# Kernel optimization log

Hardware: AMD Instinct MI355X
Metric: run time of the kernel (lower is better)

## Reference

```python
import jax, jax.numpy as jnp
import numpy as np

D, H, L, FF, V, B, S = 512, 8, 6, 2048, 4096, 2, 4096
EPS = 1e-5

def _unit(v):
    return v / jnp.linalg.norm(v, axis=-1, keepdims=True)

def _unitelu(v):
    return jax.nn.elu(_unit(v))

def _ln(x, g, b):
    m = jnp.mean(x, axis=-1, keepdims=True)
    var = jnp.var(x, axis=-1, keepdims=True)
    return (x - m) * jax.lax.rsqrt(var + EPS) * g + b

def setup_inputs() -> dict:
    key = jax.random.key(0)
    ks = jax.random.split(key, 16)
    s = 0.02
    inp = {
        'input': jax.random.randint(ks[0], (B, S), 0, V),
        'emb': jax.random.normal(ks[1], (V, D)) * s,
        'Wq': jax.random.normal(ks[2], (L, D, D)) * s,
        'bq': jnp.zeros((L, D)),
        'Wk': jax.random.normal(ks[3], (L, D, D)) * s,
        'bk': jnp.zeros((L, D)),
        'Wv': jax.random.normal(ks[4], (L, D, D)) * s,
        'bv': jnp.zeros((L, D)),
        'Wo': jax.random.normal(ks[5], (L, D, D)) * s,
        'bo': jnp.zeros((L, D)),
        'W1': jax.random.normal(ks[6], (L, FF, D)) * s,
        'b1': jnp.zeros((L, FF)),
        'W2': jax.random.normal(ks[7], (L, D, FF)) * s,
        'b2': jnp.zeros((L, D)),
        'g2': jnp.ones((L, D)),
        'be2': jnp.zeros((L, D)),
        'Wfc': jax.random.normal(ks[8], (V, D)) * s,
        'bfc': jnp.zeros((V,)),
    }
    return inp

def reference(input, emb, Wq, bq, Wk, bk, Wv, bv, Wo, bo, W1, b1, W2, b2, g2, be2, Wfc, bfc):
    # h: [S, B, D] (seq-major, matching input.permute(1,0) then embedding)
    h = emb[input.T]
    for l in range(L):
        # linear kernelized attention: O(S * dh^2) per head, no SxS matrix
        k = _unitelu((h @ Wk[l].T + bk[l]).reshape(S, B, H, -1))  # [S,B,H,dh]
        v = (h @ Wv[l].T + bv[l]).reshape(S, B, H, -1)
        A = jnp.einsum('sbnq,sbnv->bnvq', k, v)                    # [B,H,dh,dh]
        q = _unit((h @ Wq[l].T + bq[l]).reshape(S, B, H, -1))
        o = jnp.einsum('sbnq,bnvq->sbnv', q, A).reshape(S, B, D)
        h = h + (o @ Wo[l].T + bo[l])
        f = jax.nn.relu(h @ W1[l].T + b1[l]) @ W2[l].T + b2[l]
        h = _ln(h + f, g2[l], be2[l])
    out = h @ Wfc.T + bfc          # [S, B, V]
    return out.transpose(1, 2, 0)  # [B, V, S]
```

## Files before the change

kernel.cpp:

```cpp
#include <hip/hip_runtime.h>
#include <hip/hip_bf16.h>

#define D_  512
#define H_  8
#define DH_ 64
#define L_  6
#define FF_ 2048
#define V_  4096
#define B_  2
#define S_  4096
#define SB_ (S_*B_)
#define DD_ ((size_t)D_*D_)
#define FD_ ((size_t)FF_*D_)
#define NTOT_ (4*DD_ + 2*FD_)

typedef unsigned short u16;
typedef unsigned int   u32;
typedef _Float16 f16;
typedef f16   f16x8 __attribute__((ext_vector_type(8)));
typedef float f32x4 __attribute__((ext_vector_type(4)));

__device__ __forceinline__ float us2f(u16 u){
  union { u32 i; float f; } c; c.i = ((u32)u) << 16; return c.f;
}
__device__ __forceinline__ u16 f2b(float f){
  union { float f; u32 i; } c; c.f = f;
  u32 x = c.i;
  x += 0x7FFF + ((x >> 16) & 1);
  return (u16)(x >> 16);
}
__device__ __forceinline__ float h2f(u16 u){
  union { u16 s; f16 h; } c; c.s = u; return (float)c.h;
}
__device__ __forceinline__ u16 f2h(float f){
  union { f16 h; u16 s; } c; c.h = (f16)f; return c.s;
}
__device__ __forceinline__ float ldf(const void* p, size_t i, int isbf){
  return isbf ? us2f(((const u16*)p)[i]) : ((const float*)p)[i];
}

typedef const __attribute__((address_space(1))) u32* gas_u32p;
typedef       __attribute__((address_space(3))) u32* las_u32p;
__device__ __forceinline__ void async16(const u16* g, u16* l){
  __builtin_amdgcn_global_load_lds((gas_u32p)(const void*)g, (las_u32p)(void*)l, 16, 0, 0);
}

__global__ __launch_bounds__(64) void detect_dtype(const void* emb, int* flag)
{
  const int t = threadIdx.x;
  u16 hw = ((const u16*)emb)[t];
  int e = (hw >> 7) & 0xFF;
  int ok = ((e > 96) && (e < 160)) || ((hw & 0x7FFF) == 0);
  unsigned long long m = __ballot(ok);
  if (t == 0) *flag = (__popcll(m) >= 56) ? 1 : 0;
}

__global__ __launch_bounds__(256) void cvt_all(
    const void* Wq, const void* Wk, const void* Wv, const void* Wo,
    const void* W1, const void* W2, const void* Wfc,
    u16* __restrict__ dstAll, u16* __restrict__ dstFC, const int* flagp)
{
  const int isbf = *flagp;
  const size_t total6 = 6 * NTOT_;
  const size_t i = ((size_t)blockIdx.x * 256 + threadIdx.x) * 4;
  const void* src; size_t off; u16* dst;
  if (i < total6) {
    const int l = (int)(i / NTOT_);
    const size_t r = i - (size_t)l * NTOT_;
    const size_t n4 = 4 * DD_, nW1 = n4 + FD_;
    if (r < n4) {
      const int wsel = (int)(r / DD_);
      src = (wsel == 0) ? Wq : (wsel == 1) ? Wk : (wsel == 2) ? Wv : Wo;
      off = (size_t)l * DD_ + (r - (size_t)wsel * DD_);
    } else if (r < nW1) { src = W1; off = (size_t)l * FD_ + (r - n4); }
    else                { src = W2; off = (size_t)l * FD_ + (r - nW1); }
    dst = dstAll + i;
  } else {
    const size_t j = i - total6;
    if (j >= (size_t)V_ * D_) return;
    src = Wfc; off = j; dst = dstFC + j;
  }
  ushort4 o;
  if (isbf) {
    ushort4 u = *(const ushort4*)((const u16*)src + off);
    o = make_ushort4(f2h(us2f(u.x)), f2h(us2f(u.y)), f2h(us2f(u.z)), f2h(us2f(u.w)));
  } else {
    float4 f = *(const float4*)((const float*)src + off);
    o = make_ushort4(f2h(f.x), f2h(f.y), f2h(f.z), f2h(f.w));
  }
  *(ushort4*)dst = o;
}

template<int ACT, int OUTMODE, int PRE>
__global__ __launch_bounds__(256) void gemm_mfma(
    const u16* __restrict__ A, const u16* __restrict__ Bm,
    int bstride, int boff,
    const void* bias, size_t bias_off,
    const float* __restrict__ res,
    float* __restrict__ Cf, u16* __restrict__ Cb,
    void* __restrict__ Cout,
    int M, int N, int K, const int* flagp)
{
  __shared__ u16 tile[(PRE + 1) * 8192];
  const int t = threadIdx.x, lane = t & 63, w = t >> 6;
  const int bm = blockIdx.y << 7, bn = blockIdx.x << 7;
  const int bz = blockIdx.z;
  const int wr = w >> 1, wc = w & 1;
  const int col = lane & 15, quad = lane >> 4;

  const int srow = w * 16 + (lane >> 2);
  const int skol = (((lane & 3) ^ ((lane >> 3) & 3)) << 3);
  const u16* ag0 = A + (size_t)(bm + srow) * K + skol;
  const u16* ag1 = A + (size_t)(bm + 64 + srow) * K + skol;
  const u16* bg0 = Bm + ((size_t)(bn + srow) * bstride + boff + bz) * K + skol;
  const u16* bg1 = Bm + ((size_t)(bn + 64 + srow) * bstride + boff + bz) * K + skol;
  u16* la0 = &tile[       w * 512];
  u16* la1 = &tile[2048 + w * 512];
  u16* lb0 = &tile[4096 + w * 512];
  u16* lb1 = &tile[6144 + w * 512];

  const int nt = K >> 5;

  #pragma unroll
  for (int p = 0; p < PRE; ++p) {
    const int k0 = p << 5, bo = p * 8192;
    async16(ag0 + k0, la0 + bo);
    async16(ag1 + k0, la1 + bo);
    async16(bg0 + k0, lb0 + bo);
    async16(bg1 + k0, lb1 + bo);
  }
  if      (PRE >= 3) asm volatile("s_waitcnt vmcnt(8)" ::: "memory");
  else if (PRE == 2) asm volatile("s_waitcnt vmcnt(4)" ::: "memory");
  else               asm volatile("s_waitcnt vmcnt(0)" ::: "memory");
  __builtin_amdgcn_s_barrier();
  asm volatile("" ::: "memory");

  const int rswz = ((col >> 1) & 3);

  f32x4 acc[4][4] = {};
  for (int t2 = 0; t2 < nt; ++t2) {
    if (t2 + PRE < nt) {
      const int k0 = (t2 + PRE) << 5;
      const int bo = ((t2 + PRE) % (PRE + 1)) * 8192;
      async16(ag0 + k0, la0 + bo);
      async16(ag1 + k0, la1 + bo);
      async16(bg0 + k0, lb0 + bo);
      async16(bg1 + k0, lb1 + bo);
    }
    const int cur = (t2 % (PRE + 1)) * 8192;
    f16x8 af[4], bf[4];
    #pragma unroll
    for (int i = 0; i < 4; i++)
      af[i] = *(const f16x8*)&tile[cur + (wr * 64 + i * 16 + col) * 32 + ((quad ^ rswz) * 8)];
    #pragma unroll
    for (int j = 0; j < 4; j++)
      bf[j] = *(const f16x8*)&tile[cur + 4096 + (wc * 64 + j * 16 + col) * 32 + ((quad ^ rswz) * 8)];
    #pragma unroll
    for (int i = 0; i < 4; i++)
      #pragma unroll
      for (int j = 0; j < 4; j++)
        acc[i][j] = __builtin_amdgcn_mfma_f32_16x16x32_f16(af[i], bf[j], acc[i][j], 0, 0, 0);
    if (PRE >= 3) {
      if      (t2 + 3 < nt) asm volatile("s_waitcnt vmcnt(8)" ::: "memory");
      else if (t2 + 2 < nt) asm volatile("s_waitcnt vmcnt(4)" ::: "memory");
      else                  asm volatile("s_waitcnt vmcnt(0)" ::: "memory");
    } else if (PRE == 2) {
      if (t2 + 2 < nt) asm volatile("s_waitcnt vmcnt(4)" ::: "memory");
      else             asm volatile("s_waitcnt vmcnt(0)" ::: "memory");
    } else {
      asm volatile("s_waitcnt vmcnt(0)" ::: "memory");
    }
    __builtin_amdgcn_s_barrier();
    asm volatile("" ::: "memory");
  }

  const int isbf = *flagp;
  #pragma unroll
  for (int i = 0; i < 4; i++) {
    #pragma unroll
    for (int r = 0; r < 4; r++) {
      const int m = bm + wr * 64 + i * 16 + quad * 4 + r;
      #pragma unroll
      for (int j = 0; j < 4; j++) {
        const int n = bn + wc * 64 + j * 16 + col;
        float c = acc[i][j][r];
        if (OUTMODE == 3) c += ldf(bias, bias_off + m, isbf);
        else              c += ldf(bias, bias_off + n, isbf);
        if (res) c += res[(size_t)m * N + n];
        if (ACT == 1) c = fmaxf(c, 0.f);
        if (OUTMODE == 0) {
          Cb[(size_t)m * N + n] = f2h(c);
        } else if (OUTMODE == 1) {
          Cf[(size_t)m * N + n] = c;
          Cb[(size_t)m * N + n] = f2h(c);
        } else {
          const size_t oi = (size_t)bz * M * N + (size_t)m * N + n;
          if (isbf) ((u16*)Cout)[oi] = f2b(c);
          else      ((float*)Cout)[oi] = c;
        }
      }
    }
  }
}

template<int ACT, int OUTMODE, int PRE>
__global__ __launch_bounds__(256) void gemm_mfma64(
    const u16* __restrict__ A, const u16* __restrict__ Bm,
    const void* bias, size_t bias_off,
    const float* __restrict__ res,
    float* __restrict__ Cf, u16* __restrict__ Cb,
    int M, int N, int K, const int* flagp)
{
  __shared__ u16 tile[(PRE + 1) * 6144];
  const int t = threadIdx.x, lane = t & 63, w = t >> 6;
  const int bm = blockIdx.y << 6, bn = blockIdx.x << 7;
  const int wr = w >> 1, wc = w & 1;
  const int col = lane & 15, quad = lane >> 4;

  const int srow = w * 16 + (lane >> 2);
  const int skol = (((lane & 3) ^ ((lane >> 3) & 3)) << 3);
  const u16* ag  = A + (size_t)(bm + srow) * K + skol;
  const u16* bg0 = Bm + (size_t)(bn + srow) * K + skol;
  const u16* bg1 = Bm + (size_t)(bn + 64 + srow) * K + skol;
  u16* la  = &tile[       w * 512];
  u16* lb0 = &tile[2048 + w * 512];
  u16* lb1 = &tile[4096 + w * 512];

  const int nt = K >> 5;

  #pragma unroll
  for (int p = 0; p < PRE; ++p) {
    const int k0 = p << 5, bo = p * 6144;
    async16(ag  + k0, la  + bo);
    async16(bg0 + k0, lb0 + bo);
    async16(bg1 + k0, lb1 + bo);
  }
  if      (PRE >= 3) asm volatile("s_waitcnt vmcnt(6)" ::: "memory");
  else if (PRE == 2) asm volatile("s_waitcnt vmcnt(3)" ::: "memory");
  else               asm volatile("s_waitcnt vmcnt(0)" ::: "memory");
  __builtin_amdgcn_s_barrier();
  asm volatile("" ::: "memory");

  const int rswz = ((col >> 1) & 3);

  f32x4 acc[2][4] = {};
  for (int t2 = 0; t2 < nt; ++t2) {
    if (t2 + PRE < nt) {
      const int k0 = (t2 + PRE) << 5;
      const int bo = ((t2 + PRE) % (PRE + 1)) * 6144;
      async16(ag  + k0, la  + bo);
      async16(bg0 + k0, lb0 + bo);
      async16(bg1 + k0, lb1 + bo);
    }
    const int cur = (t2 % (PRE + 1)) * 6144;
    f16x8 af[2], bf[4];
    #pragma unroll
    for (int i = 0; i < 2; i++)
      af[i] = *(const f16x8*)&tile[cur + (wr * 32 + i * 16 + col) * 32 + ((quad ^ rswz) * 8)];
    #pragma unroll
    for (int j = 0; j < 4; j++)
      bf[j] = *(const f16x8*)&tile[cur + 2048 + (wc * 64 + j * 16 + col) * 32 + ((quad ^ rswz) * 8)];
    #pragma unroll
    for (int i = 0; i < 2; i++)
      #pragma unroll
      for (int j = 0; j < 4; j++)
        acc[i][j] = __builtin_amdgcn_mfma_f32_16x16x32_f16(af[i], bf[j], acc[i][j], 0, 0, 0);
    if (PRE >= 3) {
      if      (t2 + 3 < nt) asm volatile("s_waitcnt vmcnt(6)" ::: "memory");
      else if (t2 + 2 < nt) asm volatile("s_waitcnt vmcnt(3)" ::: "memory");
      else                  asm volatile("s_waitcnt vmcnt(0)" ::: "memory");
    } else if (PRE == 2) {
      if (t2 + 2 < nt) asm volatile("s_waitcnt vmcnt(3)" ::: "memory");
      else             asm volatile("s_waitcnt vmcnt(0)" ::: "memory");
    } else {
      asm volatile("s_waitcnt vmcnt(0)" ::: "memory");
    }
    __builtin_amdgcn_s_barrier();
    asm volatile("" ::: "memory");
  }

  const int isbf = *flagp;
  #pragma unroll
  for (int i = 0; i < 2; i++) {
    #pragma unroll
    for (int r = 0; r < 4; r++) {
      const int m = bm + wr * 32 + i * 16 + quad * 4 + r;
      #pragma unroll
      for (int j = 0; j < 4; j++) {
        const int n = bn + wc * 64 + j * 16 + col;
        float c = acc[i][j][r] + ldf(bias, bias_off + n, isbf);
        if (res) c += res[(size_t)m * N + n];
        if (ACT == 1) c = fmaxf(c, 0.f);
        if (OUTMODE == 0) {
          Cb[(size_t)m * N + n] = f2h(c);
        } else {
          Cf[(size_t)m * N + n] = c;
          Cb[(size_t)m * N + n] = f2h(c);
        }
      }
    }
  }
}

__global__ __launch_bounds__(256) void gemm_qkv(
    const u16* __restrict__ A, const u16* __restrict__ Bm,
    const void* bq, const void* bk, const void* bv, size_t b_off,
    u16* __restrict__ qb, u16* __restrict__ kb, u16* __restrict__ vb,
    int K, const int* flagp)
{
  __shared__ u16 tile[3 * 8192];
  const int t = threadIdx.x, lane = t & 63, w = t >> 6;
  const int bm = blockIdx.y << 7, bn = blockIdx.x << 7;
  const int wr = w >> 1, wc = w & 1;
  const int col = lane & 15, quad = lane >> 4;

  const int srow = w * 16 + (lane >> 2);
  const int skol = (((lane & 3) ^ ((lane >> 3) & 3)) << 3);
  const u16* ag0 = A + (size_t)(bm + srow) * K + skol;
  const u16* ag1 = A + (size_t)(bm + 64 + srow) * K + skol;
  const u16* bg0 = Bm + (size_t)(bn + srow) * K + skol;
  const u16* bg1 = Bm + (size_t)(bn + 64 + srow) * K + skol;
  u16* la0 = &tile[       w * 512];
  u16* la1 = &tile[2048 + w * 512];
  u16* lb0 = &tile[4096 + w * 512];
  u16* lb1 = &tile[6144 + w * 512];

  const int nt = K >> 5;

  #pragma unroll
  for (int p = 0; p < 2; ++p) {
    const int k0 = p << 5, bo = p * 8192;
    async16(ag0 + k0, la0 + bo);
    async16(ag1 + k0, la1 + bo);
    async16(bg0 + k0, lb0 + bo);
    async16(bg1 + k0, lb1 + bo);
  }
  asm volatile("s_waitcnt vmcnt(4)" ::: "memory");
  __builtin_amdgcn_s_barrier();
  asm volatile("" ::: "memory");

  const int rswz = ((col >> 1) & 3);

  f32x4 acc[4][4] = {};
  for (int t2 = 0; t2 < nt; ++t2) {
    if (t2 + 2 < nt) {
      const int k0 = (t2 + 2) << 5;
      const int bo = ((t2 + 2) % 3) * 8192;
      async16(ag0 + k0, la0 + bo);
      async16(ag1 + k0, la1 + bo);
      async16(bg0 + k0, lb0 + bo);
      async16(bg1 + k0, lb1 + bo);
    }
    const int cur = (t2 % 3) * 8192;
    f16x8 af[4], bf[4];
    #pragma unroll
    for (int i = 0; i < 4; i++)
      af[i] = *(const f16x8*)&tile[cur + (wr * 64 + i * 16 + col) * 32 + ((quad ^ rswz) * 8)];
    #pragma unroll
    for (int j = 0; j < 4; j++)
      bf[j] = *(const f16x8*)&tile[cur + 4096 + (wc * 64 + j * 16 + col) * 32 + ((quad ^ rswz) * 8)];
    #pragma unroll
    for (int i = 0; i < 4; i++)
      #pragma unroll
      for (int j = 0; j < 4; j++)
        acc[i][j] = __builtin_amdgcn_mfma_f32_16x16x32_f16(af[i], bf[j], acc[i][j], 0, 0, 0);
    if (t2 + 2 < nt) asm volatile("s_waitcnt vmcnt(4)" ::: "memory");
    else             asm volatile("s_waitcnt vmcnt(0)" ::: "memory");
    __builtin_amdgcn_s_barrier();
    asm volatile("" ::: "memory");
  }

  const int isbf = *flagp;
  const int nbase = bn + wc * 64;
  const int sel = nbase >> 9;
  const int nl0 = nbase & 511;
  u16* outp = (sel == 0) ? qb : (sel == 1) ? kb : vb;
  const void* bias = (sel == 0) ? bq : (sel == 1) ? bk : bv;

  if (sel < 2) {
    #pragma unroll
    for (int i = 0; i < 4; i++) {
      #pragma unroll
      for (int r = 0; r < 4; r++) {
        float v[4]; float ss = 0.f;
        #pragma unroll
        for (int j = 0; j < 4; j++) {
          const int nl = nl0 + j * 16 + col;
          v[j] = acc[i][j][r] + ldf(bias, b_off + nl, isbf);
          ss += v[j] * v[j];
        }
        ss += __shfl_xor(ss, 1); ss += __shfl_xor(ss, 2);
        ss += __shfl_xor(ss, 4); ss += __shfl_xor(ss, 8);
        const float inv = rsqrtf(fmaxf(ss, 1e-30f));
        const int m = bm + wr * 64 + i * 16 + quad * 4 + r;
        #pragma unroll
        for (int j = 0; j < 4; j++) {
          float u = v[j] * inv;
          if (sel == 1) u = (u > 0.f) ? u : expm1f(u);
          outp[(size_t)m * 512 + nl0 + j * 16 + col] = f2h(u);
        }
      }
    }
  } else {
    #pragma unroll
    for (int i = 0; i < 4; i++)
      #pragma unroll
      for (int r = 0; r < 4; r++) {
        const int m = bm + wr * 64 + i * 16 + quad * 4 + r;
        #pragma unroll
        for (int j = 0; j < 4; j++) {
          const int nl = nl0 + j * 16 + col;
          outp[(size_t)m * 512 + nl] = f2h(acc[i][j][r] + ldf(bias, b_off + nl, isbf));
        }
      }
  }
}

#define KT_ 136
__global__ __launch_bounds__(256) void attn_acc_mfma(
    const u16* __restrict__ kbuf, const u16* __restrict__ vbuf,
    float* __restrict__ Apart)
{
  __shared__ u16 ktr[64 * KT_];
  __shared__ u16 vtr[64 * KT_];
  const int bh = blockIdx.x;
  const int b  = bh >> 3, n = bh & 7;
  const int s0 = blockIdx.y << 7;
  const int t = threadIdx.x, lane = t & 63, w = t >> 6;
  const int col = lane & 15, quad = lane >> 4;

  #pragma unroll
  for (int u = 0; u < 8; u++) {
    const int flat = u * 256 + t;
    const int row = flat >> 4, q4 = (flat & 15) << 2;
    const size_t g = ((size_t)(s0 + row) * B_ + b) * D_ + n * 64 + q4;
    ushort4 kk = *(const ushort4*)&kbuf[g];
    ushort4 vv = *(const ushort4*)&vbuf[g];
    ktr[(q4+0)*KT_ + row] = kk.x; ktr[(q4+1)*KT_ + row] = kk.y;
    ktr[(q4+2)*KT_ + row] = kk.z; ktr[(q4+3)*KT_ + row] = kk.w;
    vtr[(q4+0)*KT_ + row] = vv.x; vtr[(q4+1)*KT_ + row] = vv.y;
    vtr[(q4+2)*KT_ + row] = vv.z; vtr[(q4+3)*KT_ + row] = vv.w;
  }
  __syncthreads();

  f32x4 acc[4] = {};
  #pragma unroll
  for (int ks = 0; ks < 4; ks++) {
    const int k0 = ks * 32;
    f16x8 af = *(const f16x8*)&vtr[(w * 16 + col) * KT_ + k0 + quad * 8];
    #pragma unroll
    for (int j = 0; j < 4; j++) {
      f16x8 bf = *(const f16x8*)&ktr[(j * 16 + col) * KT_ + k0 + quad * 8];
      acc[j] = __builtin_amdgcn_mfma_f32_16x16x32_f16(af, bf, acc[j], 0, 0, 0);
    }
  }
  float* Ap = Apart + ((size_t)blockIdx.y * 16 + bh) * 4096;
  #pragma unroll
  for (int j = 0; j < 4; j++)
    #pragma unroll
    for (int r = 0; r < 4; r++) {
      const int vi = w * 16 + quad * 4 + r, qi = j * 16 + col;
      Ap[vi * 64 + qi] = acc[j][r];
    }
}

__global__ __launch_bounds__(256) void reduce_A(
    const float* __restrict__ Apart, u16* __restrict__ Ah)
{
  const int i = blockIdx.x * 256 + threadIdx.x;
  const int bh = i >> 12, idx = i & 4095;
  float s = 0.f;
  #pragma unroll
  for (int p = 0; p < 32; p++)
    s += Apart[((size_t)p * 16 + bh) * 4096 + idx];
  Ah[i] = f2h(s);
}

__global__ __launch_bounds__(256) void attn_apply_mfma(
    u16* __restrict__ qo, const u16* __restrict__ Ah)
{
  const int bh = blockIdx.x;
  const int b = bh >> 3, n = bh & 7;
  const int s0 = blockIdx.y << 7;
  const int t = threadIdx.x, lane = t & 63, w = t >> 6;
  const int col = lane & 15, quad = lane >> 4;

  const u16* Ab_ = Ah + (size_t)bh * 4096;
  f16x8 bf[4][2];
  #pragma unroll
  for (int j = 0; j < 4; j++)
    #pragma unroll
    for (int ks = 0; ks < 2; ks++)
      bf[j][ks] = *(const f16x8*)&Ab_[(j * 16 + col) * 64 + ks * 32 + quad * 8];

  const int srow_base = s0 + w * 32;
  f32x4 acc[2][4] = {};
  #pragma unroll
  for (int i = 0; i < 2; i++) {
    const int s = srow_base + i * 16 + col;
    const u16* qp = qo + ((size_t)s * B_ + b) * D_ + n * 64;
    f16x8 af0 = *(const f16x8*)&qp[quad * 8];
    f16x8 af1 = *(const f16x8*)&qp[32 + quad * 8];
    #pragma unroll
    for (int j = 0; j < 4; j++) {
      acc[i][j] = __builtin_amdgcn_mfma_f32_16x16x32_f16(af0, bf[j][0], acc[i][j], 0, 0, 0);
      acc[i][j] = __builtin_amdgcn_mfma_f32_16x16x32_f16(af1, bf[j][1], acc[i][j], 0, 0, 0);
    }
  }
  #pragma unroll
  for (int i = 0; i < 2; i++)
    #pragma unroll
    for (int r = 0; r < 4; r++) {
      const int s = srow_base + i * 16 + quad * 4 + r;
      u16* op = qo + ((size_t)s * B_ + b) * D_ + n * 64;
      #pragma unroll
      for (int j = 0; j < 4; j++)
        op[j * 16 + col] = f2h(acc[i][j][r]);
    }
}

__global__ __launch_bounds__(256) void ln_k(
    float* __restrict__ h, u16* __restrict__ hb,
    const void* g, size_t g_off, const void* be, size_t be_off, const int* flagp)
{
  const int isbf = *flagp;
  const int m = blockIdx.x, t = threadIdx.x;
  float* p = h + (size_t)m * D_;
  const float x0 = p[t], x1 = p[t + 256];
  __shared__ float red[4];
  float s = x0 + x1;
  #pragma unroll
  for (int off = 32; off >= 1; off >>= 1) s += __shfl_xor(s, off);
  if ((t & 63) == 0) red[t >> 6] = s;
  __syncthreads();
  const float mean = (red[0] + red[1] + red[2] + red[3]) * (1.f / 512.f);
  const float d0 = x0 - mean, d1 = x1 - mean;
  float s2 = d0 * d0 + d1 * d1;
  #pragma unroll
  for (int off = 32; off >= 1; off >>= 1) s2 += __shfl_xor(s2, off);
  __syncthreads();
  if ((t & 63) == 0) red[t >> 6] = s2;
  __syncthreads();
  const float var = (red[0] + red[1] + red[2] + red[3]) * (1.f / 512.f);
  const float sc = rsqrtf(var + 1e-5f);
  const float y0 = d0 * sc * ldf(g, g_off + t, isbf)       + ldf(be, be_off + t, isbf);
  const float y1 = d1 * sc * ldf(g, g_off + t + 256, isbf) + ldf(be, be_off + t + 256, isbf);
  p[t] = y0;       p[t + 256] = y1;
  hb[(size_t)m * D_ + t] = f2h(y0);
  hb[(size_t)m * D_ + t + 256] = f2h(y1);
}

__global__ __launch_bounds__(512) void embed_k(
    const int* __restrict__ inp, const void* emb,
    float* __restrict__ h, u16* __restrict__ hb, const int* flagp)
{
  const int isbf = *flagp;
  const int m = blockIdx.x, t = threadIdx.x;
  const int s = m >> 1, b = m & 1;
  const int tok = inp[b * S_ + s];
  const float v = ldf(emb, (size_t)tok * D_ + t, isbf);
  h[(size_t)m * D_ + t] = v;
  hb[(size_t)m * D_ + t] = f2h(v);
}

extern "C" void kernel_launch(void* const* d_in, const int* in_sizes, int n_in,
                              void* d_out, int out_size, void* d_ws, size_t ws_size,
                              hipStream_t stream) {
  const int*  inp = (const int*) d_in[0];
  const void* emb = d_in[1];
  const void* Wq  = d_in[2];
  const void* bq  = d_in[3];
  const void* Wk  = d_in[4];
  const void* bk  = d_in[5];
  const void* Wv  = d_in[6];
  const void* bv  = d_in[7];
  const void* Wo  = d_in[8];
  const void* bo  = d_in[9];
  const void* W1  = d_in[10];
  const void* b1  = d_in[11];
  const void* W2  = d_in[12];
  const void* b2  = d_in[13];
  const void* g2  = d_in[14];
  const void* be2 = d_in[15];
  const void* Wfc = d_in[16];
  const void* bfc = d_in[17];

  char* ws = (char*)d_ws;
  float* h     = (float*)(ws);
  u16*   hb    = (u16*)  (ws + 16777216);
  u16*   qb    = (u16*)  (ws + 25165824);
  u16*   kb    = (u16*)  (ws + 33554432);
  u16*   vb    = (u16*)  (ws + 41943040);
  u16*   mid   = qb;
  float* Apart = (float*)(ws + 58720256);
  u16*   Ah16  = (u16*)  (ws + 67108864);
  u16*   WcAll = (u16*)  (ws + 67239936);
  u16*   WcFC  = (u16*)  (ws + 104988672);
  int*   flag  = (int*)  (ws + 109182976);

  detect_dtype<<<1, 64, 0, stream>>>(emb, flag);
  cvt_all<<<20480, 256, 0, stream>>>(Wq, Wk, Wv, Wo, W1, W2, Wfc, WcAll, WcFC, flag);
  embed_k<<<SB_, 512, 0, stream>>>(inp, emb, h, hb, flag);

  const dim3 gQ64(D_ / 128, SB_ / 64);
  const dim3 gQKV(3 * D_ / 128, SB_ / 128);
  const dim3 gF(FF_ / 128, SB_ / 128);
  const dim3 gFC(S_ / 128, V_ / 128, 2);
  const dim3 gAT(B_ * H_, S_ / 128);

  for (int l = 0; l < L_; l++) {
    u16* Wcl = WcAll + (size_t)l * NTOT_;

    gemm_qkv<<<gQKV, 256, 0, stream>>>(hb, Wcl, bq, bk, bv, (size_t)l*D_, qb, kb, vb, D_, flag);

    attn_acc_mfma<<<gAT, 256, 0, stream>>>(kb, vb, Apart);
    reduce_A<<<256, 256, 0, stream>>>(Apart, Ah16);
    attn_apply_mfma<<<gAT, 256, 0, stream>>>(qb, Ah16);

    gemm_mfma64<0,1,3><<<gQ64, 256, 0, stream>>>(qb, Wcl + 3*DD_, bo, (size_t)l*D_, h, h, hb, SB_, D_, D_, flag);
    gemm_mfma<1,0,2><<<gF, 256, 0, stream>>>(hb, Wcl + 4*DD_, 1, 0, b1, (size_t)l*FF_, nullptr, nullptr, mid, nullptr, SB_, FF_, D_, flag);
    gemm_mfma64<0,1,3><<<gQ64, 256, 0, stream>>>(mid, Wcl + 4*DD_ + FD_, b2, (size_t)l*D_, h, h, hb, SB_, D_, FF_, flag);
    ln_k<<<SB_, 256, 0, stream>>>(h, hb, g2, (size_t)l*D_, be2, (size_t)l*D_, flag);
  }

  gemm_mfma<0,3,2><<<gFC, 256, 0, stream>>>(WcFC, hb, 2, 0, bfc, 0, nullptr, nullptr, nullptr, d_out, V_, S_, D_, flag);
}
```

Measured before the change: 1.443 ms.

## Make FFN-up and final FC GEMMs persistent with cross-tile prefetch pipeline

Replaces the per-tile GEMM with a persistent variant in which each of 512 blocks handles several consecutive 128x128 output tiles. The async global-to-LDS prefetch pipeline runs continuously across tile boundaries, so the load prologue and drain are paid once per block instead of once per tile, and bias values are preloaded into registers. It also adds a mode to the FF2 GEMM that skips writing the half-precision copy of h, since layer norm regenerates it. The cost is fewer, longer blocks, an epilogue that sits inside the main loop, and higher register pressure from the bias arrays.

```diff
diff --git a/kernel.cpp b/kernel.cpp
--- a/kernel.cpp
+++ b/kernel.cpp
@@ -91,63 +91,79 @@
   *(ushort4*)dst = o;
 }
 
-template<int ACT, int OUTMODE, int PRE>
-__global__ __launch_bounds__(256) void gemm_mfma(
+template<int ACT, int OUTMODE, int PRE, int TPB, int LOG_TX, int LOG_TXZ>
+__global__ __launch_bounds__(256) void gemm_pers(
     const u16* __restrict__ A, const u16* __restrict__ Bm,
-    int bstride, int boff,
+    int bstride,
     const void* bias, size_t bias_off,
-    const float* __restrict__ res,
-    float* __restrict__ Cf, u16* __restrict__ Cb,
-    void* __restrict__ Cout,
+    u16* __restrict__ Cb, void* __restrict__ Cout,
     int M, int N, int K, const int* flagp)
 {
   __shared__ u16 tile[(PRE + 1) * 8192];
   const int t = threadIdx.x, lane = t & 63, w = t >> 6;
-  const int bm = blockIdx.y << 7, bn = blockIdx.x << 7;
-  const int bz = blockIdx.z;
   const int wr = w >> 1, wc = w & 1;
   const int col = lane & 15, quad = lane >> 4;
-
   const int srow = w * 16 + (lane >> 2);
   const int skol = (((lane & 3) ^ ((lane >> 3) & 3)) << 3);
-  const u16* ag0 = A + (size_t)(bm + srow) * K + skol;
-  const u16* ag1 = A + (size_t)(bm + 64 + srow) * K + skol;
-  const u16* bg0 = Bm + ((size_t)(bn + srow) * bstride + boff + bz) * K + skol;
-  const u16* bg1 = Bm + ((size_t)(bn + 64 + srow) * bstride + boff + bz) * K + skol;
-  u16* la0 = &tile[       w * 512];
-  u16* la1 = &tile[2048 + w * 512];
-  u16* lb0 = &tile[4096 + w * 512];
-  u16* lb1 = &tile[6144 + w * 512];
-
-  const int nt = K >> 5;
-
-  #pragma unroll
-  for (int p = 0; p < PRE; ++p) {
-    const int k0 = p << 5, bo = p * 8192;
-    async16(ag0 + k0, la0 + bo);
-    async16(ag1 + k0, la1 + bo);
-    async16(bg0 + k0, lb0 + bo);
-    async16(bg1 + k0, lb1 + bo);
-  }
-  if      (PRE >= 3) asm volatile("s_waitcnt vmcnt(8)" ::: "memory");
-  else if (PRE == 2) asm volatile("s_waitcnt vmcnt(4)" ::: "memory");
-  else               asm volatile("s_waitcnt vmcnt(0)" ::: "memory");
+  const int rswz = ((col >> 1) & 3);
+  const int isbf = *flagp;
+  const int vbase = blockIdx.x * TPB;
+
+  float bpre3[(OUTMODE == 3) ? 16 : 1];
+  float bpre0[(OUTMODE == 3) ? 1 : TPB][4];
+  if (OUTMODE == 3) {
+    const int by0 = vbase >> LOG_TXZ;
+    #pragma unroll
+    for (int i = 0; i < 4; i++)
+      #pragma unroll
+      for (int r = 0; r < 4; r++)
+        bpre3[i * 4 + r] = ldf(bias, bias_off + (by0 << 7) + wr * 64 + i * 16 + quad * 4 + r, isbf);
+  } else {
+    #pragma unroll
+    for (int g = 0; g < TPB; g++) {
+      const int bxg = (vbase + g) & ((1 << LOG_TX) - 1);
+      #pragma unroll
+      for (int j = 0; j < 4; j++)
+        bpre0[g][j] = ldf(bias, bias_off + (bxg << 7) + wc * 64 + j * 16 + col, isbf);
+    }
+  }
+
+  int st = -1;
+  const u16 *ag0 = nullptr, *ag1 = nullptr, *bg0 = nullptr, *bg1 = nullptr;
+  auto set_tile = [&](int tp) {
+    const int v  = vbase + tp;
+    const int by = v >> LOG_TXZ;
+    const int rr = v & ((1 << LOG_TXZ) - 1);
+    const int bz = rr >> LOG_TX;
+    const int bx = rr & ((1 << LOG_TX) - 1);
+    ag0 = A + (size_t)((by << 7) + srow) * K + skol;
+    ag1 = ag0 + (size_t)64 * K;
+    bg0 = Bm + ((size_t)((bx << 7) + srow) * bstride + bz) * K + skol;
+    bg1 = bg0 + (size_t)64 * bstride * K;
+  };
+  auto stage = [&](int u) {
+    const int tp = u >> 4;
+    if (tp != st) { st = tp; set_tile(tp); }
+    const int k0 = (u & 15) << 5;
+    const int bo = (u % (PRE + 1)) * 8192;
+    async16(ag0 + k0, &tile[bo +        w * 512]);
+    async16(ag1 + k0, &tile[bo + 2048 + w * 512]);
+    async16(bg0 + k0, &tile[bo + 4096 + w * 512]);
+    async16(bg1 + k0, &tile[bo + 6144 + w * 512]);
+  };
+
+  const int U = TPB * 16;
+  #pragma unroll
+  for (int p = 0; p < PRE; ++p) stage(p);
+  if (PRE >= 2) asm volatile("s_waitcnt vmcnt(4)" ::: "memory");
+  else          asm volatile("s_waitcnt vmcnt(0)" ::: "memory");
   __builtin_amdgcn_s_barrier();
   asm volatile("" ::: "memory");
 
-  const int rswz = ((col >> 1) & 3);
-
   f32x4 acc[4][4] = {};
-  for (int t2 = 0; t2 < nt; ++t2) {
-    if (t2 + PRE < nt) {
-      const int k0 = (t2 + PRE) << 5;
-      const int bo = ((t2 + PRE) % (PRE + 1)) * 8192;
-      async16(ag0 + k0, la0 + bo);
-      async16(ag1 + k0, la1 + bo);
-      async16(bg0 + k0, lb0 + bo);
-      async16(bg1 + k0, lb1 + bo);
-    }
-    const int cur = (t2 % (PRE + 1)) * 8192;
+  for (int u = 0; u < U; ++u) {
+    if (u + PRE < U) stage(u + PRE);
+    const int cur = (u % (PRE + 1)) * 8192;
     f16x8 af[4], bf[4];
     #pragma unroll
     for (int i = 0; i < 4; i++)
@@ -160,46 +176,58 @@
       #pragma unroll
       for (int j = 0; j < 4; j++)
         acc[i][j] = __builtin_amdgcn_mfma_f32_16x16x32_f16(af[i], bf[j], acc[i][j], 0, 0, 0);
-    if (PRE >= 3) {
-      if      (t2 + 3 < nt) asm volatile("s_waitcnt vmcnt(8)" ::: "memory");
-      else if (t2 + 2 < nt) asm volatile("s_waitcnt vmcnt(4)" ::: "memory");
-      else                  asm volatile("s_waitcnt vmcnt(0)" ::: "memory");
-    } else if (PRE == 2) {
-      if (t2 + 2 < nt) asm volatile("s_waitcnt vmcnt(4)" ::: "memory");
-      else             asm volatile("s_waitcnt vmcnt(0)" ::: "memory");
-    } else {
-      asm volatile("s_waitcnt vmcnt(0)" ::: "memory");
-    }
+
+    if ((u & 15) == 15) {
+      const int v  = vbase + (u >> 4);
+      const int by = v >> LOG_TXZ;
+      const int rr = v & ((1 << LOG_TXZ) - 1);
+      const int bz = rr >> LOG_TX;
+      const int bx = rr & ((1 << LOG_TX) - 1);
+      const int bm = by << 7, bn = bx << 7;
+      if (OUTMODE == 3) {
+        const size_t obase = (size_t)bz * M * N;
+        #pragma unroll
+        for (int i = 0; i < 4; i++)
+          #pragma unroll
+          for (int r = 0; r < 4; r++) {
+            const int m = bm + wr * 64 + i * 16 + quad * 4 + r;
+            #pragma unroll
+            for (int j = 0; j < 4; j++) {
+              const int n = bn + wc * 64 + j * 16 + col;
+              const float c = acc[i][j][r] + bpre3[i * 4 + r];
+              const size_t oi = obase + (size_t)m * N + n;
+              if (isbf) ((u16*)Cout)[oi] = f2b(c);
+              else      ((float*)Cout)[oi] = c;
+            }
+          }
+      } else {
+        const int g = u >> 4;
+        #pragma unroll
+        for (int i = 0; i < 4; i++)
+          #pragma unroll
+          for (int r = 0; r < 4; r++) {
+            const int m = bm + wr * 64 + i * 16 + quad * 4 + r;
+            #pragma unroll
+            for (int j = 0; j < 4; j++) {
+              const int n = bn + wc * 64 + j * 16 + col;
+              float c = acc[i][j][r] + bpre0[g][j];
+              if (ACT == 1) c = fmaxf(c, 0.f);
+              Cb[(size_t)m * N + n] = f2h(c);
+            }
+          }
+      }
+      const f32x4 z = {0.f, 0.f, 0.f, 0.f};
+      #pragma unroll
+      for (int i = 0; i < 4; i++)
+        #pragma unroll
+        for (int j = 0; j < 4; j++)
+          acc[i][j] = z;
+    }
+
+    if (PRE >= 2 && u + 2 < U) asm volatile("s_waitcnt vmcnt(4)" ::: "memory");
+    else                       asm volatile("s_waitcnt vmcnt(0)" ::: "memory");
     __builtin_amdgcn_s_barrier();
     asm volatile("" ::: "memory");
-  }
-
-  const int isbf = *flagp;
-  #pragma unroll
-  for (int i = 0; i < 4; i++) {
-    #pragma unroll
-    for (int r = 0; r < 4; r++) {
-      const int m = bm + wr * 64 + i * 16 + quad * 4 + r;
-      #pragma unroll
-      for (int j = 0; j < 4; j++) {
-        const int n = bn + wc * 64 + j * 16 + col;
-        float c = acc[i][j][r];
-        if (OUTMODE == 3) c += ldf(bias, bias_off + m, isbf);
-        else              c += ldf(bias, bias_off + n, isbf);
-        if (res) c += res[(size_t)m * N + n];
-        if (ACT == 1) c = fmaxf(c, 0.f);
-        if (OUTMODE == 0) {
-          Cb[(size_t)m * N + n] = f2h(c);
-        } else if (OUTMODE == 1) {
-          Cf[(size_t)m * N + n] = c;
-          Cb[(size_t)m * N + n] = f2h(c);
-        } else {
-          const size_t oi = (size_t)bz * M * N + (size_t)m * N + n;
-          if (isbf) ((u16*)Cout)[oi] = f2b(c);
-          else      ((float*)Cout)[oi] = c;
-        }
-      }
-    }
   }
 }
 
@@ -293,9 +321,11 @@
         if (ACT == 1) c = fmaxf(c, 0.f);
         if (OUTMODE == 0) {
           Cb[(size_t)m * N + n] = f2h(c);
+        } else if (OUTMODE == 1) {
+          Cf[(size_t)m * N + n] = c;
+          Cb[(size_t)m * N + n] = f2h(c);
         } else {
           Cf[(size_t)m * N + n] = c;
-          Cb[(size_t)m * N + n] = f2h(c);
         }
       }
     }
@@ -604,8 +634,6 @@
 
   const dim3 gQ64(D_ / 128, SB_ / 64);
   const dim3 gQKV(3 * D_ / 128, SB_ / 128);
-  const dim3 gF(FF_ / 128, SB_ / 128);
-  const dim3 gFC(S_ / 128, V_ / 128, 2);
   const dim3 gAT(B_ * H_, S_ / 128);
 
   for (int l = 0; l < L_; l++) {
@@ -618,10 +646,10 @@
     attn_apply_mfma<<<gAT, 256, 0, stream>>>(qb, Ah16);
 
     gemm_mfma64<0,1,3><<<gQ64, 256, 0, stream>>>(qb, Wcl + 3*DD_, bo, (size_t)l*D_, h, h, hb, SB_, D_, D_, flag);
-    gemm_mfma<1,0,2><<<gF, 256, 0, stream>>>(hb, Wcl + 4*DD_, 1, 0, b1, (size_t)l*FF_, nullptr, nullptr, mid, nullptr, SB_, FF_, D_, flag);
-    gemm_mfma64<0,1,3><<<gQ64, 256, 0, stream>>>(mid, Wcl + 4*DD_ + FD_, b2, (size_t)l*D_, h, h, hb, SB_, D_, FF_, flag);
+    gemm_pers<1,0,2,2,4,4><<<512, 256, 0, stream>>>(hb, Wcl + 4*DD_, 1, b1, (size_t)l*FF_, mid, nullptr, SB_, FF_, D_, flag);
+    gemm_mfma64<0,2,3><<<gQ64, 256, 0, stream>>>(mid, Wcl + 4*DD_ + FD_, b2, (size_t)l*D_, h, h, nullptr, SB_, D_, FF_, flag);
     ln_k<<<SB_, 256, 0, stream>>>(h, hb, g2, (size_t)l*D_, be2, (size_t)l*D_, flag);
   }
 
-  gemm_mfma<0,3,2><<<gFC, 256, 0, stream>>>(WcFC, hb, 2, 0, bfc, 0, nullptr, nullptr, nullptr, d_out, V_, S_, D_, flag);
-}
+  gemm_pers<0,3,2,4,5,6><<<512, 256, 0, stream>>>(WcFC, hb, 2, bfc, 0, nullptr, d_out, V_, S_, D_, flag);
+}
```

New measurement: 1.345 ms. -6.8%, faster.
